# Kernel optimization log

Measured on AMD Instinct MI355X. Metric: run time of the kernel, lower is better.

The kernel has to match this reference:

```python
import jax, jax.numpy as jnp
import numpy as np

HEADS = 16  # matches init_kwargs


def setup_inputs() -> dict:
    key = jax.random.key(0)
    ks = jax.random.split(key, 9)
    N, L, E, D = 2, 2048, 1024, 64
    return {
        "query": jax.random.normal(ks[0], (N, L, E), dtype=jnp.float32),
        "keys": jax.random.normal(ks[1], (N, L, E), dtype=jnp.float32),
        "values": jax.random.normal(ks[2], (N, L, E), dtype=jnp.float32),
        "masks": jax.random.randint(ks[3], (N, 1, 1, L), 0, 2, dtype=jnp.int32),
        "Wq": jax.random.normal(ks[4], (D, D), dtype=jnp.float32) / np.sqrt(D),
        "Wk": jax.random.normal(ks[5], (D, D), dtype=jnp.float32) / np.sqrt(D),
        "Wv": jax.random.normal(ks[6], (D, D), dtype=jnp.float32) / np.sqrt(D),
        "Wo": jax.random.normal(ks[7], (E, E), dtype=jnp.float32) / np.sqrt(E),
        "bo": jax.random.normal(ks[8], (E,), dtype=jnp.float32),
    }


def reference(query, keys, values, masks, Wq, Wk, Wv, Wo, bo):
    N, Lq, E = query.shape
    Lk = keys.shape[1]
    H = HEADS
    D = E // H
    # split heads: [N, L, H, D]
    q = query.reshape(N, Lq, H, D)
    k = keys.reshape(N, Lk, H, D)
    v = values.reshape(N, Lk, H, D)
    # per-head linear projections (weights shared across heads); Linear: x @ W.T
    q = jnp.einsum("nqhd,ed->nqhe", q, Wq)
    k = jnp.einsum("nkhd,ed->nkhe", k, Wk)
    v = jnp.einsum("nkhd,ed->nkhe", v, Wv)
    # scores [N, H, Lq, Lk]
    scores = jnp.einsum("nqhd,nkhd->nhqk", q, k)
    scores = jnp.where(masks == 0, jnp.float32(-1e20), scores)
    # NOTE: original scales by sqrt(embed_size), not sqrt(head_dim)
    attn = jax.nn.softmax(scores / jnp.sqrt(jnp.float32(E)), axis=3)
    out = jnp.einsum("nhqk,nkhd->nqhd", attn, v).reshape(N, Lq, E)
    return out @ Wo.T + bo
```

## Files before the change

kernel.cpp:

```cpp
#include <hip/hip_runtime.h>


typedef __bf16 bf16_t;
typedef __bf16 bf16x4 __attribute__((ext_vector_type(4)));
typedef __bf16 bf16x8 __attribute__((ext_vector_type(8)));
typedef float f32x4 __attribute__((ext_vector_type(4)));

#define MFMA16(a, b, c) __builtin_amdgcn_mfma_f32_16x16x32_bf16((a), (b), (c), 0, 0, 0)

#define GLOAD_LDS16(gp, lp)                                              \
    __builtin_amdgcn_global_load_lds(                                    \
        (const __attribute__((address_space(1))) void*)(gp),             \
        (__attribute__((address_space(3))) void*)(lp), 16, 0, 0)

__device__ inline bf16x8 cvt8(const float* __restrict__ p, float scale) {
    f32x4 a = *(const f32x4*)p;
    f32x4 b = *(const f32x4*)(p + 4);
    bf16x8 r;
    r[0] = (bf16_t)(a[0] * scale); r[1] = (bf16_t)(a[1] * scale);
    r[2] = (bf16_t)(a[2] * scale); r[3] = (bf16_t)(a[3] * scale);
    r[4] = (bf16_t)(b[0] * scale); r[5] = (bf16_t)(b[1] * scale);
    r[6] = (bf16_t)(b[2] * scale); r[7] = (bf16_t)(b[3] * scale);
    return r;
}

__global__ __launch_bounds__(256) void scan_kernel(const int* __restrict__ msk,
                                                   int* __restrict__ excl)
{
    __shared__ int sums[256];
    const int t = threadIdx.x;
    for (int n = 0; n < 2; n++) {
        const int* m = msk + n * 2048;
        int* e = excl + n * 2049;
        int v[8], s = 0;
        #pragma unroll
        for (int j = 0; j < 8; j++) { v[j] = (m[t * 8 + j] != 0); s += v[j]; }
        sums[t] = s;
        __syncthreads();
        if (t == 0) {
            int a = 0;
            for (int i = 0; i < 256; i++) { int x = sums[i]; sums[i] = a; a += x; }
            e[2048] = a;
        }
        __syncthreads();
        int a = sums[t];
        #pragma unroll
        for (int j = 0; j < 8; j++) { e[t * 8 + j] = a; a += v[j]; }
        __syncthreads();
    }
}

__global__ __launch_bounds__(256) void qkv_proj_kernel(
    const float* __restrict__ qin, const float* __restrict__ kin,
    const float* __restrict__ vin,
    const float* __restrict__ Wq, const float* __restrict__ Wk,
    const float* __restrict__ Wv, const float* __restrict__ Wo,
    const int* __restrict__ excl,
    bf16_t* __restrict__ qp, bf16_t* __restrict__ kc, bf16_t* __restrict__ vcT,
    bf16_t* __restrict__ Wob)
{
    __shared__ __align__(16) char smem[51200];

    const int t = threadIdx.x;
    const int w = t >> 6, lane = t & 63, quad = lane >> 4, l16 = lane & 15;

    if (blockIdx.y == 3) {
        int idx = blockIdx.x * 1024 + t * 4;
        f32x4 v = *(const f32x4*)&Wo[idx];
        bf16x4 r;
        r[0] = (bf16_t)v[0]; r[1] = (bf16_t)v[1];
        r[2] = (bf16_t)v[2]; r[3] = (bf16_t)v[3];
        *(bf16x4*)&Wob[idx] = r;
        return;
    }

    if (blockIdx.y == 2) {
        bf16_t* Ct = (bf16_t*)smem;
        short* mapS = (short*)(smem + 16384);
        const int h = blockIdx.x & 15;
        const int tb = (blockIdx.x >> 4) * 64;
        const int n = tb >> 11, l0 = tb & 2047;
        const int tg = tb + w * 16 + l16;

        bf16x8 b0 = cvt8(&vin[(size_t)tg * 1024 + h * 64 + quad * 8], 1.0f);
        bf16x8 b1 = cvt8(&vin[(size_t)tg * 1024 + h * 64 + 32 + quad * 8], 1.0f);

        const int cbase = excl[n * 2049 + l0];
        const int cnt   = excl[n * 2049 + l0 + 64] - cbase;
        if (t < 64) {
            int c  = excl[n * 2049 + l0 + t];
            int c1 = excl[n * 2049 + l0 + t + 1];
            if (c1 > c) mapS[c - cbase] = (short)t;
        }

        #pragma unroll
        for (int nt = 0; nt < 4; nt++) {
            bf16x8 a0 = cvt8(&Wv[(nt * 16 + l16) * 64 + quad * 8], 1.0f);
            bf16x8 a1 = cvt8(&Wv[(nt * 16 + l16) * 64 + 32 + quad * 8], 1.0f);
            f32x4 acc = {0.f, 0.f, 0.f, 0.f};
            acc = MFMA16(a0, b0, acc);
            acc = MFMA16(a1, b1, acc);
            #pragma unroll
            for (int r = 0; r < 4; r++)
                Ct[(nt * 16 + quad * 4 + r) * 72 + w * 16 + l16] = (bf16_t)acc[r];
        }
        __syncthreads();
        const int p = t & 63, rg = t >> 6;
        if (p < cnt) {
            int j = mapS[p];
            size_t ob = ((size_t)(n * 16 + h)) * 131072 + cbase + p;
            #pragma unroll
            for (int rr = 0; rr < 16; rr++) {
                int r = rg * 16 + rr;
                vcT[ob + (size_t)r * 2048] = Ct[r * 72 + j];
            }
        }
        return;
    }

    if (blockIdx.x >= 512) return;
    const bool isK = (blockIdx.y == 1);
    const float* x; const float* W; float scale;
    if (!isK) { x = qin; W = Wq; scale = 0.03125f; }
    else      { x = kin; W = Wk; scale = 1.0f; }

    float* Xs = (float*)smem;
    bf16_t* Ct2 = (bf16_t*)(smem + 32768);

    const int g0 = blockIdx.x * 128;

    #pragma unroll
    for (int j = 0; j < 8; j++) {
        int br = w * 32 + j * 4;
        GLOAD_LDS16(&x[(size_t)(g0 + br) * 64 + lane * 4], &Xs[br * 64]);
    }
    __syncthreads();

    const int rbase = w * 32;
    bf16x8 a[2][2];
    #pragma unroll
    for (int qs = 0; qs < 2; qs++)
        #pragma unroll
        for (int c = 0; c < 2; c++)
            a[qs][c] = cvt8(&Xs[(rbase + qs * 16 + l16) * 64 + c * 32 + quad * 8], scale);

    f32x4 acc[4][2];
    #pragma unroll
    for (int nt = 0; nt < 4; nt++) {
        bf16x8 b0 = cvt8(&W[(nt * 16 + l16) * 64 + quad * 8], 1.0f);
        bf16x8 b1 = cvt8(&W[(nt * 16 + l16) * 64 + 32 + quad * 8], 1.0f);
        #pragma unroll
        for (int qs = 0; qs < 2; qs++) {
            f32x4 z = {0.f, 0.f, 0.f, 0.f};
            z = MFMA16(a[qs][0], b0, z);
            z = MFMA16(a[qs][1], b1, z);
            acc[nt][qs] = z;
        }
    }

    #pragma unroll
    for (int nt = 0; nt < 4; nt++)
        #pragma unroll
        for (int qs = 0; qs < 2; qs++)
            #pragma unroll
            for (int r = 0; r < 4; r++)
                Ct2[(rbase + qs * 16 + quad * 4 + r) * 72 + nt * 16 + l16] = (bf16_t)acc[nt][qs][r];
    __syncthreads();

    #pragma unroll
    for (int it = 0; it < 4; it++) {
        int j = it * 32 + (t >> 3);
        int g = g0 + j, h2 = g & 15, token = g >> 4;
        int n2 = token >> 11, l = token & 2047;
        bf16x8 val = *(const bf16x8*)&Ct2[j * 72 + (t & 7) * 8];
        if (isK) {
            int c  = excl[n2 * 2049 + l];
            int c1 = excl[n2 * 2049 + l + 1];
            if (c1 > c)
                *(bf16x8*)&kc[(((size_t)(n2 * 16 + h2)) * 2048 + c) * 64 + (t & 7) * 8] = val;
        } else {
            *(bf16x8*)&qp[(((size_t)(n2 * 16 + h2)) * 2048 + l) * 64 + (t & 7) * 8] = val;
        }
    }
}

__global__ __launch_bounds__(256) void attn_kernel(
    const bf16_t* __restrict__ qp, const bf16_t* __restrict__ kc,
    const bf16_t* __restrict__ vcT, const int* __restrict__ excl,
    bf16_t* __restrict__ ao)
{
    __shared__ bf16_t Kt[2][64][64];
    __shared__ bf16_t Vt[2][64][64];
    __shared__ bf16_t PwT[4][32][72];

    const int t = threadIdx.x;
    const int w = t >> 6, lane = t & 63, quad = lane >> 4, l16 = lane & 15;

    const int flat = blockIdx.x;
    const int xcd = flat & 7, slot = flat >> 3;
    const int nh = xcd * 4 + (slot >> 4), qb = slot & 15;
    const int n = nh >> 4, h = nh & 15;
    const int qbase = qb * 128 + w * 32;
    const size_t nhbase = (size_t)nh * 131072;

    const int Lc = excl[n * 2049 + 2048];
    const int ntiles = (Lc + 63) >> 6;

    bf16x8 aq[2][2];
    #pragma unroll
    for (int qs = 0; qs < 2; qs++)
        #pragma unroll
        for (int c = 0; c < 2; c++)
            aq[qs][c] = *(const bf16x8*)&qp[nhbase + (size_t)(qbase + qs * 16 + l16) * 64 + c * 32 + quad * 8];

    f32x4 o[2][4];
    float lsum[2] = {0.f, 0.f};
    #pragma unroll
    for (int qs = 0; qs < 2; qs++)
        #pragma unroll
        for (int dt = 0; dt < 4; dt++) {
            o[qs][dt][0] = 0.f; o[qs][dt][1] = 0.f; o[qs][dt][2] = 0.f; o[qs][dt][3] = 0.f;
        }

    const int kwbase = w * 16;

    #pragma unroll
    for (int j = 0; j < 2; j++) {
        int rb = kwbase + j * 8;
        GLOAD_LDS16(&kc[nhbase + (size_t)rb * 64 + lane * 8], &Kt[0][rb][0]);
        GLOAD_LDS16(&vcT[nhbase + (size_t)(rb + (lane >> 3)) * 2048 + (lane & 7) * 8],
                    &Vt[0][rb][0]);
    }

    for (int i = 0; i < ntiles; i++) {
        const int cb = i & 1, nb = cb ^ 1;
        const int k0 = i * 64;
        __syncthreads();

        if (i + 1 < ntiles) {
            const int kn = k0 + 64;
            #pragma unroll
            for (int j = 0; j < 2; j++) {
                int rb = kwbase + j * 8;
                GLOAD_LDS16(&kc[nhbase + (size_t)(kn + rb) * 64 + lane * 8], &Kt[nb][rb][0]);
                GLOAD_LDS16(&vcT[nhbase + (size_t)(rb + (lane >> 3)) * 2048 + kn + (lane & 7) * 8],
                            &Vt[nb][rb][0]);
            }
        }

        f32x4 st[2][4];
        #pragma unroll
        for (int ct = 0; ct < 4; ct++) {
            bf16x8 kb0 = *(const bf16x8*)&Kt[cb][ct * 16 + l16][quad * 8];
            bf16x8 kb1 = *(const bf16x8*)&Kt[cb][ct * 16 + l16][32 + quad * 8];
            #pragma unroll
            for (int qs = 0; qs < 2; qs++) {
                f32x4 acc = {0.f, 0.f, 0.f, 0.f};
                acc = MFMA16(kb0, aq[qs][0], acc);
                acc = MFMA16(kb1, aq[qs][1], acc);
                st[qs][ct] = acc;
            }
        }

        if (k0 + 64 <= Lc) {
            #pragma unroll
            for (int ct = 0; ct < 4; ct++)
                #pragma unroll
                for (int qs = 0; qs < 2; qs++) {
                    bf16x4 pk;
                    #pragma unroll
                    for (int r = 0; r < 4; r++) {
                        float p = __expf(st[qs][ct][r]);
                        lsum[qs] += p;
                        pk[r] = (bf16_t)p;
                    }
                    *(bf16x4*)&PwT[w][qs * 16 + l16][ct * 16 + quad * 4] = pk;
                }
        } else {
            #pragma unroll
            for (int ct = 0; ct < 4; ct++)
                #pragma unroll
                for (int qs = 0; qs < 2; qs++) {
                    bf16x4 pk;
                    #pragma unroll
                    for (int r = 0; r < 4; r++) {
                        int kk = k0 + ct * 16 + quad * 4 + r;
                        float p = (kk < Lc) ? __expf(st[qs][ct][r]) : 0.0f;
                        lsum[qs] += p;
                        pk[r] = (bf16_t)p;
                    }
                    *(bf16x4*)&PwT[w][qs * 16 + l16][ct * 16 + quad * 4] = pk;
                }
        }
        asm volatile("s_waitcnt lgkmcnt(0)" ::: "memory");

        bf16x8 bp[2][2];
        #pragma unroll
        for (int qs = 0; qs < 2; qs++) {
            bp[qs][0] = *(const bf16x8*)&PwT[w][qs * 16 + l16][quad * 8];
            bp[qs][1] = *(const bf16x8*)&PwT[w][qs * 16 + l16][32 + quad * 8];
        }
        #pragma unroll
        for (int dt = 0; dt < 4; dt++) {
            bf16x8 va0 = *(const bf16x8*)&Vt[cb][dt * 16 + l16][quad * 8];
            bf16x8 va1 = *(const bf16x8*)&Vt[cb][dt * 16 + l16][32 + quad * 8];
            #pragma unroll
            for (int qs = 0; qs < 2; qs++) {
                o[qs][dt] = MFMA16(va0, bp[qs][0], o[qs][dt]);
                o[qs][dt] = MFMA16(va1, bp[qs][1], o[qs][dt]);
            }
        }
    }

    #pragma unroll
    for (int qs = 0; qs < 2; qs++) {
        float v = lsum[qs];
        v += __shfl_xor(v, 16);
        v += __shfl_xor(v, 32);
        float inv = 1.0f / v;
        const int q = qbase + qs * 16 + l16;
        const size_t base = ((size_t)n * 2048 + q) * 1024 + h * 64;
        #pragma unroll
        for (int dt = 0; dt < 4; dt++) {
            bf16x4 ov;
            #pragma unroll
            for (int r = 0; r < 4; r++) ov[r] = (bf16_t)(o[qs][dt][r] * inv);
            *(bf16x4*)&ao[base + dt * 16 + quad * 4] = ov;
        }
    }
}

__global__ __launch_bounds__(256, 2) void out_proj_kernel(
    const bf16_t* __restrict__ X, const bf16_t* __restrict__ Wob,
    const float* __restrict__ bo, float* __restrict__ out)
{
    __shared__ bf16_t Xs[2][128][64];
    __shared__ bf16_t Ws[2][64][64];

    const int t = threadIdx.x;
    const int w = t >> 6, lane = t & 63, quad = lane >> 4, l16 = lane & 15;
    const int Mbase = blockIdx.x * 128;
    const int Nbase = blockIdx.y * 64;
    const int mrow = (w & 1) * 64;
    const int ncol = (w >> 1) * 32;

    f32x4 acc[4][2];
    #pragma unroll
    for (int mi = 0; mi < 4; mi++)
        #pragma unroll
        for (int ni = 0; ni < 2; ni++) {
            acc[mi][ni][0] = 0.f; acc[mi][ni][1] = 0.f;
            acc[mi][ni][2] = 0.f; acc[mi][ni][3] = 0.f;
        }

    #pragma unroll
    for (int j = 0; j < 4; j++) {
        int br = w * 32 + j * 8;
        GLOAD_LDS16(&X[(size_t)(Mbase + br + (lane >> 3)) * 1024 + (lane & 7) * 8],
                    &Xs[0][br][0]);
    }
    #pragma unroll
    for (int j = 0; j < 2; j++) {
        int br = w * 16 + j * 8;
        GLOAD_LDS16(&Wob[(size_t)(Nbase + br + (lane >> 3)) * 1024 + (lane & 7) * 8],
                    &Ws[0][br][0]);
    }

    for (int i = 0; i < 16; i++) {
        const int cb = i & 1, nb = cb ^ 1;
        __syncthreads();

        if (i < 15) {
            const int kn = (i + 1) * 64;
            #pragma unroll
            for (int j = 0; j < 4; j++) {
                int br = w * 32 + j * 8;
                GLOAD_LDS16(&X[(size_t)(Mbase + br + (lane >> 3)) * 1024 + kn + (lane & 7) * 8],
                            &Xs[nb][br][0]);
            }
            #pragma unroll
            for (int j = 0; j < 2; j++) {
                int br = w * 16 + j * 8;
                GLOAD_LDS16(&Wob[(size_t)(Nbase + br + (lane >> 3)) * 1024 + kn + (lane & 7) * 8],
                            &Ws[nb][br][0]);
            }
        }

        #pragma unroll
        for (int c = 0; c < 2; c++) {
            bf16x8 bfr[2];
            #pragma unroll
            for (int ni = 0; ni < 2; ni++)
                bfr[ni] = *(const bf16x8*)&Ws[cb][ncol + ni * 16 + l16][c * 32 + quad * 8];
            #pragma unroll
            for (int mi = 0; mi < 4; mi++) {
                bf16x8 afr = *(const bf16x8*)&Xs[cb][mrow + mi * 16 + l16][c * 32 + quad * 8];
                #pragma unroll
                for (int ni = 0; ni < 2; ni++)
                    acc[mi][ni] = MFMA16(afr, bfr[ni], acc[mi][ni]);
            }
        }
    }

    #pragma unroll
    for (int ni = 0; ni < 2; ni++) {
        float b = bo[Nbase + ncol + ni * 16 + l16];
        #pragma unroll
        for (int mi = 0; mi < 4; mi++) {
            #pragma unroll
            for (int r = 0; r < 4; r++) {
                int row = Mbase + mrow + mi * 16 + quad * 4 + r;
                out[(size_t)row * 1024 + Nbase + ncol + ni * 16 + l16] = acc[mi][ni][r] + b;
            }
        }
    }
}

extern "C" void kernel_launch(void* const* d_in, const int* in_sizes, int n_in,
                              void* d_out, int out_size, void* d_ws, size_t ws_size,
                              hipStream_t stream)
{
    const float* qin = (const float*)d_in[0];
    const float* kin = (const float*)d_in[1];
    const float* vin = (const float*)d_in[2];
    const int*   msk = (const int*)d_in[3];
    const float* Wq  = (const float*)d_in[4];
    const float* Wk  = (const float*)d_in[5];
    const float* Wv  = (const float*)d_in[6];
    const float* Wo  = (const float*)d_in[7];
    const float* bo  = (const float*)d_in[8];
    float* out = (float*)d_out;

    bf16_t* ws  = (bf16_t*)d_ws;
    bf16_t* qp  = ws;
    bf16_t* kc  = ws + 4194304;
    bf16_t* vcT = ws + 8388608;
    bf16_t* ao  = ws + 12582912;
    bf16_t* Wob = ws + 16777216;
    int* excl   = (int*)(ws + 17825792);

    scan_kernel<<<1, 256, 0, stream>>>(msk, excl);
    qkv_proj_kernel<<<dim3(1024, 4), 256, 0, stream>>>(qin, kin, vin, Wq, Wk, Wv, Wo,
                                                        excl, qp, kc, vcT, Wob);
    attn_kernel<<<dim3(512), 256, 0, stream>>>(qp, kc, vcT, excl, ao);
    out_proj_kernel<<<dim3(32, 16), 256, 0, stream>>>(ao, Wob, bo, out);
}
```

Before: 185.2 us.

## Use 8 waves per attention block and parallelize mask prefix scan

The attention kernel now runs 512 threads per block, each wave handling 16 queries instead of 32, so each wave loads one K/V row group per tile instead of two. This raises wave-level parallelism and shortens per-wave latency chains, at the cost of reusing each K/V tile across fewer MFMA operations per wave and adding more block-wide barrier participants. The mask scan kernel switches from a serial single-thread scan to a wave shuffle scan with one block per batch, cutting launch-serial overhead.

```diff
diff --git a/kernel.cpp b/kernel.cpp
--- a/kernel.cpp
+++ b/kernel.cpp
@@ -27,27 +27,33 @@
 __global__ __launch_bounds__(256) void scan_kernel(const int* __restrict__ msk,
                                                    int* __restrict__ excl)
 {
-    __shared__ int sums[256];
-    const int t = threadIdx.x;
-    for (int n = 0; n < 2; n++) {
-        const int* m = msk + n * 2048;
-        int* e = excl + n * 2049;
-        int v[8], s = 0;
-        #pragma unroll
-        for (int j = 0; j < 8; j++) { v[j] = (m[t * 8 + j] != 0); s += v[j]; }
-        sums[t] = s;
-        __syncthreads();
-        if (t == 0) {
-            int a = 0;
-            for (int i = 0; i < 256; i++) { int x = sums[i]; sums[i] = a; a += x; }
-            e[2048] = a;
-        }
-        __syncthreads();
-        int a = sums[t];
-        #pragma unroll
-        for (int j = 0; j < 8; j++) { e[t * 8 + j] = a; a += v[j]; }
-        __syncthreads();
-    }
+    __shared__ int wsum[4];
+    const int t = threadIdx.x, lane = t & 63, w = t >> 6;
+    const int n = blockIdx.x;
+    const int* m = msk + n * 2048;
+    int* e = excl + n * 2049;
+
+    int v[8], s = 0;
+    #pragma unroll
+    for (int j = 0; j < 8; j++) { v[j] = (m[t * 8 + j] != 0); s += v[j]; }
+
+    int isc = s;
+    #pragma unroll
+    for (int d = 1; d < 64; d <<= 1) {
+        int x = __shfl_up(isc, d);
+        if (lane >= d) isc += x;
+    }
+    if (lane == 63) wsum[w] = isc;
+    __syncthreads();
+
+    int woff = 0;
+    #pragma unroll
+    for (int i = 0; i < 4; i++) if (i < w) woff += wsum[i];
+    if (t == 0) e[2048] = wsum[0] + wsum[1] + wsum[2] + wsum[3];
+
+    int a = woff + isc - s;
+    #pragma unroll
+    for (int j = 0; j < 8; j++) { e[t * 8 + j] = a; a += v[j]; }
 }
 
 __global__ __launch_bounds__(256) void qkv_proj_kernel(
@@ -184,14 +190,14 @@
     }
 }
 
-__global__ __launch_bounds__(256) void attn_kernel(
+__global__ __launch_bounds__(512) void attn_kernel(
     const bf16_t* __restrict__ qp, const bf16_t* __restrict__ kc,
     const bf16_t* __restrict__ vcT, const int* __restrict__ excl,
     bf16_t* __restrict__ ao)
 {
     __shared__ bf16_t Kt[2][64][64];
     __shared__ bf16_t Vt[2][64][64];
-    __shared__ bf16_t PwT[4][32][72];
+    __shared__ bf16_t PwT[8][16][72];
 
     const int t = threadIdx.x;
     const int w = t >> 6, lane = t & 63, quad = lane >> 4, l16 = lane & 15;
@@ -200,37 +206,27 @@
     const int xcd = flat & 7, slot = flat >> 3;
     const int nh = xcd * 4 + (slot >> 4), qb = slot & 15;
     const int n = nh >> 4, h = nh & 15;
-    const int qbase = qb * 128 + w * 32;
+    const int qbase = qb * 128 + w * 16;
     const size_t nhbase = (size_t)nh * 131072;
 
     const int Lc = excl[n * 2049 + 2048];
     const int ntiles = (Lc + 63) >> 6;
 
-    bf16x8 aq[2][2];
-    #pragma unroll
-    for (int qs = 0; qs < 2; qs++)
-        #pragma unroll
-        for (int c = 0; c < 2; c++)
-            aq[qs][c] = *(const bf16x8*)&qp[nhbase + (size_t)(qbase + qs * 16 + l16) * 64 + c * 32 + quad * 8];
-
-    f32x4 o[2][4];
-    float lsum[2] = {0.f, 0.f};
-    #pragma unroll
-    for (int qs = 0; qs < 2; qs++)
-        #pragma unroll
-        for (int dt = 0; dt < 4; dt++) {
-            o[qs][dt][0] = 0.f; o[qs][dt][1] = 0.f; o[qs][dt][2] = 0.f; o[qs][dt][3] = 0.f;
-        }
-
-    const int kwbase = w * 16;
-
-    #pragma unroll
-    for (int j = 0; j < 2; j++) {
-        int rb = kwbase + j * 8;
-        GLOAD_LDS16(&kc[nhbase + (size_t)rb * 64 + lane * 8], &Kt[0][rb][0]);
-        GLOAD_LDS16(&vcT[nhbase + (size_t)(rb + (lane >> 3)) * 2048 + (lane & 7) * 8],
-                    &Vt[0][rb][0]);
-    }
+    bf16x8 aq[2];
+    #pragma unroll
+    for (int c = 0; c < 2; c++)
+        aq[c] = *(const bf16x8*)&qp[nhbase + (size_t)(qbase + l16) * 64 + c * 32 + quad * 8];
+
+    f32x4 o[4];
+    float lsum = 0.f;
+    #pragma unroll
+    for (int dt = 0; dt < 4; dt++) { o[dt][0] = 0.f; o[dt][1] = 0.f; o[dt][2] = 0.f; o[dt][3] = 0.f; }
+
+    const int srow = w * 8;
+
+    GLOAD_LDS16(&kc[nhbase + (size_t)srow * 64 + lane * 8], &Kt[0][srow][0]);
+    GLOAD_LDS16(&vcT[nhbase + (size_t)(srow + (lane >> 3)) * 2048 + (lane & 7) * 8],
+                &Vt[0][srow][0]);
 
     for (int i = 0; i < ntiles; i++) {
         const int cb = i & 1, nb = cb ^ 1;
@@ -239,92 +235,73 @@
 
         if (i + 1 < ntiles) {
             const int kn = k0 + 64;
-            #pragma unroll
-            for (int j = 0; j < 2; j++) {
-                int rb = kwbase + j * 8;
-                GLOAD_LDS16(&kc[nhbase + (size_t)(kn + rb) * 64 + lane * 8], &Kt[nb][rb][0]);
-                GLOAD_LDS16(&vcT[nhbase + (size_t)(rb + (lane >> 3)) * 2048 + kn + (lane & 7) * 8],
-                            &Vt[nb][rb][0]);
-            }
-        }
-
-        f32x4 st[2][4];
+            GLOAD_LDS16(&kc[nhbase + (size_t)(kn + srow) * 64 + lane * 8], &Kt[nb][srow][0]);
+            GLOAD_LDS16(&vcT[nhbase + (size_t)(srow + (lane >> 3)) * 2048 + kn + (lane & 7) * 8],
+                        &Vt[nb][srow][0]);
+        }
+
+        f32x4 st[4];
         #pragma unroll
         for (int ct = 0; ct < 4; ct++) {
             bf16x8 kb0 = *(const bf16x8*)&Kt[cb][ct * 16 + l16][quad * 8];
             bf16x8 kb1 = *(const bf16x8*)&Kt[cb][ct * 16 + l16][32 + quad * 8];
-            #pragma unroll
-            for (int qs = 0; qs < 2; qs++) {
-                f32x4 acc = {0.f, 0.f, 0.f, 0.f};
-                acc = MFMA16(kb0, aq[qs][0], acc);
-                acc = MFMA16(kb1, aq[qs][1], acc);
-                st[qs][ct] = acc;
-            }
+            f32x4 acc = {0.f, 0.f, 0.f, 0.f};
+            acc = MFMA16(kb0, aq[0], acc);
+            acc = MFMA16(kb1, aq[1], acc);
+            st[ct] = acc;
         }
 
         if (k0 + 64 <= Lc) {
             #pragma unroll
-            for (int ct = 0; ct < 4; ct++)
+            for (int ct = 0; ct < 4; ct++) {
+                bf16x4 pk;
                 #pragma unroll
-                for (int qs = 0; qs < 2; qs++) {
-                    bf16x4 pk;
-                    #pragma unroll
-                    for (int r = 0; r < 4; r++) {
-                        float p = __expf(st[qs][ct][r]);
-                        lsum[qs] += p;
-                        pk[r] = (bf16_t)p;
-                    }
-                    *(bf16x4*)&PwT[w][qs * 16 + l16][ct * 16 + quad * 4] = pk;
+                for (int r = 0; r < 4; r++) {
+                    float p = __expf(st[ct][r]);
+                    lsum += p;
+                    pk[r] = (bf16_t)p;
                 }
+                *(bf16x4*)&PwT[w][l16][ct * 16 + quad * 4] = pk;
+            }
         } else {
             #pragma unroll
-            for (int ct = 0; ct < 4; ct++)
+            for (int ct = 0; ct < 4; ct++) {
+                bf16x4 pk;
                 #pragma unroll
-                for (int qs = 0; qs < 2; qs++) {
-                    bf16x4 pk;
-                    #pragma unroll
-                    for (int r = 0; r < 4; r++) {
-                        int kk = k0 + ct * 16 + quad * 4 + r;
-                        float p = (kk < Lc) ? __expf(st[qs][ct][r]) : 0.0f;
-                        lsum[qs] += p;
-                        pk[r] = (bf16_t)p;
-                    }
-                    *(bf16x4*)&PwT[w][qs * 16 + l16][ct * 16 + quad * 4] = pk;
+                for (int r = 0; r < 4; r++) {
+                    int kk = k0 + ct * 16 + quad * 4 + r;
+                    float p = (kk < Lc) ? __expf(st[ct][r]) : 0.0f;
+                    lsum += p;
+                    pk[r] = (bf16_t)p;
                 }
+                *(bf16x4*)&PwT[w][l16][ct * 16 + quad * 4] = pk;
+            }
         }
         asm volatile("s_waitcnt lgkmcnt(0)" ::: "memory");
 
-        bf16x8 bp[2][2];
-        #pragma unroll
-        for (int qs = 0; qs < 2; qs++) {
-            bp[qs][0] = *(const bf16x8*)&PwT[w][qs * 16 + l16][quad * 8];
-            bp[qs][1] = *(const bf16x8*)&PwT[w][qs * 16 + l16][32 + quad * 8];
-        }
+        bf16x8 bp0 = *(const bf16x8*)&PwT[w][l16][quad * 8];
+        bf16x8 bp1 = *(const bf16x8*)&PwT[w][l16][32 + quad * 8];
         #pragma unroll
         for (int dt = 0; dt < 4; dt++) {
             bf16x8 va0 = *(const bf16x8*)&Vt[cb][dt * 16 + l16][quad * 8];
             bf16x8 va1 = *(const bf16x8*)&Vt[cb][dt * 16 + l16][32 + quad * 8];
-            #pragma unroll
-            for (int qs = 0; qs < 2; qs++) {
-                o[qs][dt] = MFMA16(va0, bp[qs][0], o[qs][dt]);
-                o[qs][dt] = MFMA16(va1, bp[qs][1], o[qs][dt]);
-            }
-        }
-    }
-
-    #pragma unroll
-    for (int qs = 0; qs < 2; qs++) {
-        float v = lsum[qs];
+            o[dt] = MFMA16(va0, bp0, o[dt]);
+            o[dt] = MFMA16(va1, bp1, o[dt]);
+        }
+    }
+
+    {
+        float v = lsum;
         v += __shfl_xor(v, 16);
         v += __shfl_xor(v, 32);
         float inv = 1.0f / v;
-        const int q = qbase + qs * 16 + l16;
+        const int q = qbase + l16;
         const size_t base = ((size_t)n * 2048 + q) * 1024 + h * 64;
         #pragma unroll
         for (int dt = 0; dt < 4; dt++) {
             bf16x4 ov;
             #pragma unroll
-            for (int r = 0; r < 4; r++) ov[r] = (bf16_t)(o[qs][dt][r] * inv);
+            for (int r = 0; r < 4; r++) ov[r] = (bf16_t)(o[dt][r] * inv);
             *(bf16x4*)&ao[base + dt * 16 + quad * 4] = ov;
         }
     }
@@ -439,9 +416,9 @@
     bf16_t* Wob = ws + 16777216;
     int* excl   = (int*)(ws + 17825792);
 
-    scan_kernel<<<1, 256, 0, stream>>>(msk, excl);
+    scan_kernel<<<dim3(2), 256, 0, stream>>>(msk, excl);
     qkv_proj_kernel<<<dim3(1024, 4), 256, 0, stream>>>(qin, kin, vin, Wq, Wk, Wv, Wo,
                                                         excl, qp, kc, vcT, Wob);
-    attn_kernel<<<dim3(512), 256, 0, stream>>>(qp, kc, vcT, excl, ao);
+    attn_kernel<<<dim3(512), 512, 0, stream>>>(qp, kc, vcT, excl, ao);
     out_proj_kernel<<<dim3(32, 16), 256, 0, stream>>>(ao, Wob, bo, out);
 }
```

New measurement: 191.7 us. +3.5%, slower.
